# Kernel optimization log

Hardware: AMD Instinct MI355X
Metric: run time of the kernel (lower is better)

Reference implementation:

```python
import jax, jax.numpy as jnp
import numpy as np
from jax import lax

B, DIM, H, W = 2, 128, 192, 192
GS = [16, 32, 32, 48]          # group ratios [1,2,2,3]/8 of DIM
HID = int(DIM * 2.66)          # 340, Restormer-style hidden width


def _pool_mat(n_in, n_out):
    # torch AdaptiveAvgPool as an explicit linear map [n_out, n_in]
    P = np.zeros((n_out, n_in), np.float32)
    for o in range(n_out):
        s = (o * n_in) // n_out
        e = ((o + 1) * n_in + n_out - 1) // n_out
        P[o, s:e] = 1.0 / (e - s)
    return jnp.asarray(P)


def _ln(t, w, b):
    # WithBias LayerNorm over the channel dim of NCHW (== LN over last dim of b(hw)c)
    mu = t.mean(1, keepdims=True)
    var = ((t - mu) ** 2).mean(1, keepdims=True)
    return (t - mu) / jnp.sqrt(var + 1e-5) * w[None, :, None, None] + b[None, :, None, None]


def _c1x1(t, w):
    return jnp.einsum('oc,bchw->bohw', w, t)


def _dw3(t, w):
    return lax.conv_general_dilated(t, w, (1, 1), 'SAME',
                                    dimension_numbers=('NCHW', 'OIHW', 'NCHW'),
                                    feature_group_count=t.shape[1])


def _c1d(t, w, b):
    return jnp.einsum('oc,bcl->bol', w, t) + b[None, :, None]


def _gelu(t):
    return jax.nn.gelu(t, approximate=False)


def _forward(x, qv_cache, ln1_w, ln1_b, ln2_w, ln2_b, temperature, w_qkv, w_qkv_dw, w_proj,
             intra_down_w, intra_down_b, intra_up_w, intra_up_b, intra_gate_w, intra_gate_b,
             inter0_cw_w, inter0_cw_b, inter0_g_w, inter0_g_b,
             inter1_cw_w, inter1_cw_b, inter1_g_w, inter1_g_b,
             inter2_cw_w, inter2_cw_b, inter2_g_w, inter2_g_b,
             inter3_cw_w, inter3_cw_b, inter3_g_w, inter3_g_b,
             ffn_in_w, ffn_dw_w, ffn_out_w):
    b, c, h, w_ = x.shape
    hw = h * w_
    inter_p = [(inter0_cw_w, inter0_cw_b, inter0_g_w, inter0_g_b),
               (inter1_cw_w, inter1_cw_b, inter1_g_w, inter1_g_b),
               (inter2_cw_w, inter2_cw_b, inter2_g_w, inter2_g_b),
               (inter3_cw_w, inter3_cw_b, inter3_g_w, inter3_g_b)]
    # ---- attention branch ----
    xn = _ln(x, ln1_w, ln1_b)
    qkv = _dw3(_c1x1(xn, w_qkv), w_qkv_dw)
    q, k, v = jnp.split(qkv, 3, axis=1)
    q = q.reshape(b, c, hw); k = k.reshape(b, c, hw); v = v.reshape(b, c, hw)
    # correlation-based channel re-grouping (torch.corrcoef on batch-mean of q)
    cf = q.mean(0)                                   # [C, HW]
    xm = cf - cf.mean(1, keepdims=True)
    cov = xm @ xm.T
    dsd = jnp.sqrt(jnp.diagonal(cov))
    corr = cov / (dsd[:, None] * dsd[None, :])
    idx = jnp.argsort(-corr.mean(1))                 # descending mean similarity
    q = q[:, idx]; k = k[:, idx]; v = v[:, idx]
    atts, tmpc, outs = [], [], []
    start = 0
    for i, g in enumerate(GS):
        qg = q[:, start:start + g]; kg = k[:, start:start + g]; vg = v[:, start:start + g]
        start += g
        qn = qg / jnp.maximum(jnp.linalg.norm(qg, axis=-1, keepdims=True), 1e-12)
        kn = kg / jnp.maximum(jnp.linalg.norm(kg, axis=-1, keepdims=True), 1e-12)
        att = jax.nn.softmax(jnp.einsum('bcl,bdl->bcd', qn, kn) * temperature[i, 0, 0], axis=-1)
        tmpc.append(lax.stop_gradient(qn) + lax.stop_gradient(kn))
        # Inter_CacheModulation: adaptive-pool cache to [g,g], FiLM + gated conv1d
        cw_w, cw_b, g_w, g_b = inter_p[i]
        P = _pool_mat(c, g)
        aligned = jnp.einsum('oi,bij,pj->bop', P, qv_cache, P)    # [1, g, g]
        scale, shift = jnp.split(_c1d(aligned + att, cw_w, cw_b), 2, axis=1)
        x1p = att * scale + shift
        att = x1p * _gelu(_c1d(x1p, g_w, g_b)) + att
        atts.append(att)
        outs.append(jnp.einsum('bcd,bdl->bcl', att, vg))
    # CalculateCurrentLayerCache: resize each group's batch-mean attn to [C,C].
    # Original does (u * c_i) // dim with c_i == dim, i.e. elementwise floor.
    acc = jnp.zeros((1, c, c), x.dtype)
    for a in atts:
        m = lax.stop_gradient(a).mean(0, keepdims=True)[:, None]  # [1,1,g,g]
        u = jax.image.resize(m, (1, 1, c, c), method='bilinear')
        acc = acc + jnp.floor(u)[:, 0]
    qv_new = qv_cache * 0.9 + acc * 0.1
    out_all = jnp.concatenate(outs, axis=1)          # [B, C, HW]
    tmp_all = jnp.concatenate(tmpc, axis=1)
    # Intra_CacheModulation
    s = tmp_all + out_all
    gated = _gelu(_c1d(s, intra_gate_w, intra_gate_b)) * s
    out_all = _c1d(_c1d(gated, intra_down_w, intra_down_b), intra_up_w, intra_up_b) + out_all
    x1 = x + _c1x1(out_all.reshape(b, c, h, w_), w_proj)
    # ---- gated-dconv FFN ----
    xn2 = _ln(x1, ln2_w, ln2_b)
    y1, y2 = jnp.split(_dw3(_c1x1(xn2, ffn_in_w), ffn_dw_w), 2, axis=1)
    out = x1 + _c1x1(_gelu(y1) * y2, ffn_out_w)
    return out, qv_new


def setup_inputs() -> dict:
    key = jax.random.key(0)
    ks = jax.random.split(key, 40)
    def w(i, shape, s=0.02):
        return jax.random.normal(ks[i], shape, jnp.float32) * s
    p = {}
    p['x'] = jax.random.normal(ks[0], (B, DIM, H, W), jnp.float32)
    p['qv_cache'] = jax.random.uniform(ks[1], (1, DIM, DIM), jnp.float32)
    p['ln1_w'] = jnp.ones((DIM,), jnp.float32); p['ln1_b'] = jnp.zeros((DIM,), jnp.float32)
    p['ln2_w'] = jnp.ones((DIM,), jnp.float32); p['ln2_b'] = jnp.zeros((DIM,), jnp.float32)
    p['temperature'] = jnp.ones((4, 1, 1), jnp.float32)
    p['w_qkv'] = w(2, (3 * DIM, DIM))
    p['w_qkv_dw'] = w(3, (3 * DIM, 1, 3, 3))
    p['w_proj'] = w(4, (DIM, DIM))
    p['intra_down_w'] = w(5, (DIM // 2, DIM)); p['intra_down_b'] = jnp.zeros((DIM // 2,), jnp.float32)
    p['intra_up_w'] = w(6, (DIM, DIM // 2)); p['intra_up_b'] = jnp.zeros((DIM,), jnp.float32)
    p['intra_gate_w'] = w(7, (DIM, DIM)); p['intra_gate_b'] = jnp.zeros((DIM,), jnp.float32)
    for i, g in enumerate(GS):
        p[f'inter{i}_cw_w'] = w(8 + 2 * i, (2 * g, g))
        p[f'inter{i}_cw_b'] = jnp.zeros((2 * g,), jnp.float32)
        p[f'inter{i}_g_w'] = w(9 + 2 * i, (g, g))
        p[f'inter{i}_g_b'] = jnp.zeros((g,), jnp.float32)
    p['ffn_in_w'] = w(20, (2 * HID, DIM))
    p['ffn_dw_w'] = w(21, (2 * HID, 1, 3, 3))
    p['ffn_out_w'] = w(22, (DIM, HID))
    return p


def reference(x, qv_cache, ln1_w, ln1_b, ln2_w, ln2_b, temperature, w_qkv, w_qkv_dw, w_proj,
              intra_down_w, intra_down_b, intra_up_w, intra_up_b, intra_gate_w, intra_gate_b,
              inter0_cw_w, inter0_cw_b, inter0_g_w, inter0_g_b,
              inter1_cw_w, inter1_cw_b, inter1_g_w, inter1_g_b,
              inter2_cw_w, inter2_cw_b, inter2_g_w, inter2_g_b,
              inter3_cw_w, inter3_cw_b, inter3_g_w, inter3_g_b,
              ffn_in_w, ffn_dw_w, ffn_out_w):
    return _forward(x, qv_cache, ln1_w, ln1_b, ln2_w, ln2_b, temperature, w_qkv, w_qkv_dw, w_proj,
                    intra_down_w, intra_down_b, intra_up_w, intra_up_b, intra_gate_w, intra_gate_b,
                    inter0_cw_w, inter0_cw_b, inter0_g_w, inter0_g_b,
                    inter1_cw_w, inter1_cw_b, inter1_g_w, inter1_g_b,
                    inter2_cw_w, inter2_cw_b, inter2_g_w, inter2_g_b,
                    inter3_cw_w, inter3_cw_b, inter3_g_w, inter3_g_b,
                    ffn_in_w, ffn_dw_w, ffn_out_w)
```

## Files before the change

### kernel.cpp

```cpp
#include <hip/hip_runtime.h>
#include <math.h>

#define TPB 256

constexpr int BN_  = 2;
constexpr int CDIM = 128;
constexpr int HH   = 192;
constexpr int WW   = 192;
constexpr int HWc  = HH * WW;
constexpr int C3   = 384;
constexpr int HID  = 340;
constexpr int NL2  = 288;
constexpr int CH2  = HWc / NL2;
constexpr int CV   = 288;

typedef unsigned short bf16_t;
typedef __attribute__((ext_vector_type(8))) __bf16 bf16x8;
typedef __attribute__((ext_vector_type(4))) float f32x4;

__device__ __forceinline__ float b2f(bf16_t v) {
  unsigned u = ((unsigned)v) << 16;
  return __uint_as_float(u);
}
__device__ __forceinline__ bf16_t f2b(float f) {
  unsigned u = __float_as_uint(f);
  unsigned r = (u + 0x7FFFu + ((u >> 16) & 1u)) >> 16;
  return (bf16_t)r;
}
__device__ __forceinline__ float ldf(const float* p) { return *p; }
__device__ __forceinline__ float ldf(const bf16_t* p) { return b2f(*p); }
__device__ __forceinline__ void stf(float* p, float v) { *p = v; }
__device__ __forceinline__ void stf(bf16_t* p, float v) { *p = f2b(v); }

__device__ __forceinline__ void ldv4(const float* p, float* v) {
  float4 t = *(const float4*)p;
  v[0] = t.x; v[1] = t.y; v[2] = t.z; v[3] = t.w;
}
__device__ __forceinline__ void ldv4(const bf16_t* p, float* v) {
  ushort4 t = *(const ushort4*)p;
  v[0] = b2f(t.x); v[1] = b2f(t.y); v[2] = b2f(t.z); v[3] = b2f(t.w);
}
__device__ __forceinline__ void stv4(float* p, const float* v) {
  float4 t; t.x = v[0]; t.y = v[1]; t.z = v[2]; t.w = v[3];
  *(float4*)p = t;
}
__device__ __forceinline__ void stv4(bf16_t* p, const float* v) {
  ushort4 t; t.x = f2b(v[0]); t.y = f2b(v[1]); t.z = f2b(v[2]); t.w = f2b(v[3]);
  *(ushort4*)p = t;
}

__device__ __forceinline__ float gelu_f(float x) {
  return 0.5f * x * (1.0f + erff(x * 0.7071067811865475f));
}

__device__ __forceinline__ void unpack8(uint4 v, float* rv) {
  unsigned wv[4] = {v.x, v.y, v.z, v.w};
#pragma unroll
  for (int j = 0; j < 8; ++j)
    rv[j + 1] = b2f((bf16_t)((wv[j >> 1] >> ((j & 1) * 16)) & 0xFFFFu));
}
__device__ __forceinline__ uint4 pack8(const float* a) {
  uint4 o;
  unsigned w[4];
#pragma unroll
  for (int p = 0; p < 4; ++p) {
    unsigned lo = f2b(a[2 * p]), hi = f2b(a[2 * p + 1]);
    w[p] = lo | (hi << 16);
  }
  o.x = w[0]; o.y = w[1]; o.z = w[2]; o.w = w[3];
  return o;
}
__device__ __forceinline__ float sum8(uint4 v) {
  unsigned w[4] = {v.x, v.y, v.z, v.w};
  float s = 0.f;
#pragma unroll
  for (int j = 0; j < 8; ++j)
    s += b2f((bf16_t)((w[j >> 1] >> ((j & 1) * 16)) & 0xFFFFu));
  return s;
}
__device__ __forceinline__ float sumsq8(uint4 v) {
  unsigned w[4] = {v.x, v.y, v.z, v.w};
  float s = 0.f;
#pragma unroll
  for (int j = 0; j < 8; ++j) {
    float t = b2f((bf16_t)((w[j >> 1] >> ((j & 1) * 16)) & 0xFFFFu));
    s += t * t;
  }
  return s;
}

__device__ __constant__ int dGSZ[4]   = {16, 32, 32, 48};
__device__ __constant__ int dGST[4]   = {0, 16, 48, 80};
__device__ __constant__ int dAOFF[4]  = {0, 256, 1280, 2304};
__device__ __constant__ int dABASE[4] = {0, 512, 2560, 4608};

constexpr size_t oATTRAW  = 0;
constexpr size_t oATTS2   = 65536;
constexpr size_t oMUP     = 102400;
constexpr size_t oWB      = 131072;
constexpr size_t oATTS    = 1327104;
constexpr size_t oNORMQ   = 1363968;
constexpr size_t oNORMK   = 1364992;
constexpr size_t oIDX     = 1366016;
constexpr size_t oMU      = 1366528;
constexpr size_t oCOV     = 1367040;
constexpr size_t oQKV     = 1572864;
constexpr size_t oXN      = 58195968;
constexpr size_t oOUTALL  = 77070336;
constexpr size_t oSBUF    = 95944704;
constexpr size_t WS_NEED  = 114819072;
constexpr size_t oCHUNK1  = oOUTALL;
constexpr size_t oCOVPART = oOUTALL;
constexpr size_t oCOVP2   = oSBUF;
constexpr size_t oQKPART  = oXN;
constexpr size_t oGATED   = oQKV;
constexpr size_t oDBUF    = oQKV + 18874368;
constexpr size_t oY0C     = oQKV;
constexpr size_t oZ       = oOUTALL;
constexpr size_t oX1B     = oXN;

constexpr int eWQ   = 0;
constexpr int eGATE = 49152;
constexpr int eDOWN = 65536;
constexpr int eUP   = 73728;
constexpr int ePROJ = 81920;
constexpr int eFFI  = 98304;
constexpr int eFFO  = 185344;
constexpr int eTOT  = 234496;

__global__ __launch_bounds__(TPB) void k_wcvt(const float* __restrict__ wq,
                                              const float* __restrict__ gate,
                                              const float* __restrict__ down,
                                              const float* __restrict__ up,
                                              const float* __restrict__ proj,
                                              const float* __restrict__ ffi,
                                              const float* __restrict__ ffo,
                                              bf16_t* __restrict__ wb) {
  int t = blockIdx.x * TPB + threadIdx.x;
  if (t >= eTOT) return;
  int u = t;
  if (u < 49152) { wb[eWQ + u] = f2b(wq[u]); return; }
  u -= 49152;
  if (u < 16384) { wb[eGATE + u] = f2b(gate[u]); return; }
  u -= 16384;
  if (u < 8192)  { wb[eDOWN + u] = f2b(down[u]); return; }
  u -= 8192;
  if (u < 8192)  { wb[eUP + u] = f2b(up[u]); return; }
  u -= 8192;
  if (u < 16384) { wb[ePROJ + u] = f2b(proj[u]); return; }
  u -= 16384;
  if (u < 87040) { wb[eFFI + u] = f2b(ffi[u]); return; }
  u -= 87040;
  {
    int o = u / 384, k = u - o * 384;
    wb[eFFO + u] = (k < HID) ? f2b(ffo[o * HID + k]) : (bf16_t)0;
  }
}

template <typename TI>
__global__ __launch_bounds__(TPB) void k_ln(const TI* __restrict__ x,
                                            const float* __restrict__ w,
                                            const float* __restrict__ bias,
                                            bf16_t* __restrict__ out) {
  int t = blockIdx.x * TPB + threadIdx.x;
  if (t >= BN_ * HWc) return;
  int b = t / HWc, l = t - b * HWc;
  const TI* xb = x + (size_t)b * CDIM * HWc + l;
  float s = 0.f, s2 = 0.f;
#pragma unroll 4
  for (int c = 0; c < CDIM; ++c) { float v = ldf(&xb[(size_t)c * HWc]); s += v; s2 += v * v; }
  float mu  = s * (1.f / CDIM);
  float var = s2 * (1.f / CDIM) - mu * mu;
  float inv = 1.f / sqrtf(var + 1e-5f);
  bf16_t* ob = out + (size_t)b * CDIM * HWc + l;
#pragma unroll 4
  for (int c = 0; c < CDIM; ++c)
    stf(&ob[(size_t)c * HWc], (ldf(&xb[(size_t)c * HWc]) - mu) * inv * w[c] + bias[c]);
}

template <typename TO, typename TA, int KT, int EPI>
__global__ __launch_bounds__(TPB) void k_mgA(const bf16_t* __restrict__ W,
                                             const bf16_t* __restrict__ W2, int osplit,
                                             const float* __restrict__ bias,
                                             const bf16_t* __restrict__ in,
                                             const TA* __restrict__ aux,
                                             TO* __restrict__ out, int O,
                                             int ibr, int obr, int abr) {
  constexpr int L  = HWc;
  constexpr int PK = KT + 8;
  constexpr int KH = KT / 2;
  constexpr int SH = (KT == 128) ? 6 : 5;
  __shared__ bf16_t At[128 * PK];
  __shared__ bf16_t Wt[64 * PK];
  int b = blockIdx.y;
  const bf16_t* inb  = in  + (size_t)b * ibr * L;
  const TA*     auxb = aux ? aux + (size_t)b * abr * L : nullptr;
  TO*           outb = out + (size_t)b * obr * L;
  int l0 = blockIdx.x * 128;
  int tid = threadIdx.x, lane = tid & 63, wid = tid >> 6;
  int wm = wid >> 1, wn = wid & 1;
  int cl = lane & 15, rg = lane >> 4;

#pragma unroll
  for (int r = 0; r < (KH * 16) / TPB; ++r) {
    int u  = tid + r * TPB;
    int k2 = u & (KH - 1), lb = u >> SH;
    int ka = k2 * 2;
    uint4 rowA = *(const uint4*)(&inb[(size_t)ka * L + l0 + lb * 8]);
    uint4 rowB = *(const uint4*)(&inb[(size_t)(ka + 1) * L + l0 + lb * 8]);
    unsigned wa[4] = {rowA.x, rowA.y, rowA.z, rowA.w};
    unsigned wb[4] = {rowB.x, rowB.y, rowB.z, rowB.w};
#pragma unroll
    for (int j = 0; j < 8; ++j) {
      unsigned va = (wa[j >> 1] >> ((j & 1) * 16)) & 0xFFFFu;
      unsigned vb = (wb[j >> 1] >> ((j & 1) * 16)) & 0xFFFFu;
      *(unsigned*)(&At[(lb * 8 + j) * PK + ka]) = va | (vb << 16);
    }
  }

  int noc = (O + 63) >> 6;
  for (int oc = 0; oc < noc; ++oc) {
    int o0 = oc * 64;
#pragma unroll
    for (int r = 0; r < (64 * KT / 8) / TPB; ++r) {
      int e = tid + r * TPB;
      int o = e / (KT / 8), k8 = (e % (KT / 8)) * 8;
      int og = o0 + o;
      uint4 wv = {0u, 0u, 0u, 0u};
      if (og < O) {
        const bf16_t* wrow = (og < osplit) ? (W + (size_t)og * KT)
                                           : (W2 + (size_t)(og - osplit) * KT);
        wv = *(const uint4*)(&wrow[k8]);
      }
      *(uint4*)(&Wt[o * PK + k8]) = wv;
    }
    __syncthreads();
    f32x4 acc[2][4];
#pragma unroll
    for (int m = 0; m < 2; ++m)
#pragma unroll
      for (int n = 0; n < 4; ++n) acc[m][n] = (f32x4){0.f, 0.f, 0.f, 0.f};
#pragma unroll
    for (int kk = 0; kk < KT / 32; ++kk) {
      int kof = kk * 32 + rg * 8;
      bf16x8 a[2], bfr[4];
#pragma unroll
      for (int m = 0; m < 2; ++m)
        a[m] = *(const bf16x8*)(&Wt[(wm * 32 + m * 16 + cl) * PK + kof]);
#pragma unroll
      for (int n = 0; n < 4; ++n)
        bfr[n] = *(const bf16x8*)(&At[(wn * 64 + n * 16 + cl) * PK + kof]);
#pragma unroll
      for (int m = 0; m < 2; ++m)
#pragma unroll
        for (int n = 0; n < 4; ++n)
          acc[m][n] = __builtin_amdgcn_mfma_f32_16x16x32_bf16(bfr[n], a[m], acc[m][n], 0, 0, 0);
    }
    __syncthreads();
#pragma unroll
    for (int m = 0; m < 2; ++m) {
      int og = o0 + wm * 32 + m * 16 + cl;
      if (og >= O) continue;
      float bv = bias ? bias[og] : 0.f;
#pragma unroll
      for (int n = 0; n < 4; ++n) {
        int lcol = l0 + wn * 64 + n * 16 + rg * 4;
        size_t off = (size_t)og * L + lcol;
        float v[4];
#pragma unroll
        for (int r = 0; r < 4; ++r) v[r] = acc[m][n][r] + bv;
        if (EPI == 1) {
          float a4[4]; ldv4(&auxb[off], a4);
#pragma unroll
          for (int r = 0; r < 4; ++r) v[r] += a4[r];
        } else if (EPI == 2) {
          float a4[4]; ldv4(&auxb[off], a4);
#pragma unroll
          for (int r = 0; r < 4; ++r) v[r] = gelu_f(v[r]) * a4[r];
        } else if (EPI == 3) {
          int lloc = wn * 64 + n * 16 + rg * 4;
#pragma unroll
          for (int r = 0; r < 4; ++r)
            v[r] = gelu_f(v[r]) * b2f(At[(lloc + r) * PK + og]);
        }
        stv4(&outb[off], v);
      }
    }
  }
}

template <typename TO, typename TA, int EPI>
__global__ __launch_bounds__(TPB) void k_mgB(const bf16_t* __restrict__ Wb,
                                             const float* __restrict__ bias,
                                             const bf16_t* __restrict__ in,
                                             const TA* __restrict__ aux,
                                             TO* __restrict__ out, int O, int K,
                                             int ibr, int obr, int abr) {
  constexpr int L = HWc;
  constexpr int PK = 72, BK = 64, WSTR = 384;
  __shared__ bf16_t At[128 * PK];
  __shared__ bf16_t Wt[128 * PK];
  int b = blockIdx.y;
  const bf16_t* inb  = in  + (size_t)b * ibr * L;
  const TA*     auxb = aux ? aux + (size_t)b * abr * L : nullptr;
  TO*           outb = out + (size_t)b * obr * L;
  int l0 = blockIdx.x * 128;
  int tid = threadIdx.x, lane = tid & 63, wid = tid >> 6;
  int wm = wid >> 1, wn = wid & 1;
  int cl = lane & 15, rg = lane >> 4;

  f32x4 acc[4][4];
#pragma unroll
  for (int m = 0; m < 4; ++m)
#pragma unroll
    for (int n = 0; n < 4; ++n) acc[m][n] = (f32x4){0.f, 0.f, 0.f, 0.f};

  for (int k0 = 0; k0 < K; k0 += BK) {
#pragma unroll
    for (int r = 0; r < 2; ++r) {
      int u = tid + r * TPB;
      int k2 = u & 31, lb = u >> 5;
      int ka = k0 + k2 * 2;
      uint4 rowA = {0u,0u,0u,0u}, rowB = {0u,0u,0u,0u};
      if (ka < K)     rowA = *(const uint4*)(&inb[(size_t)ka * L + l0 + lb * 8]);
      if (ka + 1 < K) rowB = *(const uint4*)(&inb[(size_t)(ka + 1) * L + l0 + lb * 8]);
      unsigned wa[4] = {rowA.x, rowA.y, rowA.z, rowA.w};
      unsigned wb[4] = {rowB.x, rowB.y, rowB.z, rowB.w};
#pragma unroll
      for (int j = 0; j < 8; ++j) {
        unsigned va = (wa[j >> 1] >> ((j & 1) * 16)) & 0xFFFFu;
        unsigned vb = (wb[j >> 1] >> ((j & 1) * 16)) & 0xFFFFu;
        *(unsigned*)(&At[(lb * 8 + j) * PK + k2 * 2]) = va | (vb << 16);
      }
    }
#pragma unroll
    for (int r = 0; r < 4; ++r) {
      int e = tid + r * TPB;
      int o = e >> 3, k8 = (e & 7) * 8;
      uint4 wv = *(const uint4*)(&Wb[(size_t)o * WSTR + k0 + k8]);
      *(uint4*)(&Wt[o * PK + k8]) = wv;
    }
    __syncthreads();
#pragma unroll
    for (int kk = 0; kk < 2; ++kk) {
      int kof = kk * 32 + rg * 8;
      bf16x8 a[4], bfr[4];
#pragma unroll
      for (int m = 0; m < 4; ++m)
        a[m] = *(const bf16x8*)(&Wt[(wm * 64 + m * 16 + cl) * PK + kof]);
#pragma unroll
      for (int n = 0; n < 4; ++n)
        bfr[n] = *(const bf16x8*)(&At[(wn * 64 + n * 16 + cl) * PK + kof]);
#pragma unroll
      for (int m = 0; m < 4; ++m)
#pragma unroll
        for (int n = 0; n < 4; ++n)
          acc[m][n] = __builtin_amdgcn_mfma_f32_16x16x32_bf16(bfr[n], a[m], acc[m][n], 0, 0, 0);
    }
    __syncthreads();
  }
#pragma unroll
  for (int m = 0; m < 4; ++m) {
    int og = wm * 64 + m * 16 + cl;
    if (og >= O) continue;
    float bv = bias ? bias[og] : 0.f;
#pragma unroll
    for (int n = 0; n < 4; ++n) {
      int lcol = l0 + wn * 64 + n * 16 + rg * 4;
      size_t off = (size_t)og * L + lcol;
      float v[4];
#pragma unroll
      for (int r = 0; r < 4; ++r) v[r] = acc[m][n][r] + bv;
      if (EPI == 1) {
        float a4[4]; ldv4(&auxb[off], a4);
#pragma unroll
        for (int r = 0; r < 4; ++r) v[r] += a4[r];
      } else if (EPI == 2) {
        float a4[4]; ldv4(&auxb[off], a4);
#pragma unroll
        for (int r = 0; r < 4; ++r) v[r] = gelu_f(v[r]) * a4[r];
      }
      stv4(&outb[off], v);
    }
  }
}

__global__ __launch_bounds__(TPB) void k_dw3v(const bf16_t* __restrict__ in,
                                              const float* __restrict__ wt,
                                              bf16_t* __restrict__ out,
                                              int Cc, int c0, int CoutTotal, long totalG) {
  long t = (long)blockIdx.x * TPB + threadIdx.x;
  if (t >= totalG) return;
  int g = (int)(t % (HWc / 8));
  long bc = t / (HWc / 8);
  int cl = (int)(bc % Cc);
  int b = (int)(bc / Cc);
  int h = g / (WW / 8), w8 = (g % (WW / 8)) * 8;
  const bf16_t* ib = in + ((size_t)b * Cc + cl) * HWc;
  const float* wc = wt + (size_t)(c0 + cl) * 9;
  float rowv[3][10];
#pragma unroll
  for (int dy = -1; dy <= 1; ++dy) {
    float* rv = rowv[dy + 1];
    int hh = h + dy;
    if ((unsigned)hh >= (unsigned)HH) {
#pragma unroll
      for (int j = 0; j < 10; ++j) rv[j] = 0.f;
      continue;
    }
    const bf16_t* rp = ib + hh * WW + w8;
    unpack8(*(const uint4*)rp, rv);
    rv[0] = (w8 > 0) ? b2f(rp[-1]) : 0.f;
    rv[9] = (w8 + 8 < WW) ? b2f(rp[8]) : 0.f;
  }
  float a[8];
#pragma unroll
  for (int j = 0; j < 8; ++j) {
    float s = 0.f;
#pragma unroll
    for (int dy = 0; dy < 3; ++dy)
#pragma unroll
      for (int dx = 0; dx < 3; ++dx)
        s += rowv[dy][j + dx] * wc[dy * 3 + dx];
    a[j] = s;
  }
  *(uint4*)(&out[((size_t)b * CoutTotal + c0 + cl) * HWc + h * WW + w8]) = pack8(a);
}

__global__ __launch_bounds__(TPB) void k_mu1(const bf16_t* __restrict__ qkv,
                                             float* __restrict__ mupart) {
  int c = blockIdx.x, ch = blockIdx.y;
  int tid = threadIdx.x;
  int base = ch * (HWc / 8);
  __shared__ float red[TPB];
  float s = 0.f;
  for (int u = tid; u < (HWc / 8) / 8; u += TPB) {
    uint4 v0 = *(const uint4*)(&qkv[(size_t)c * HWc + base + u * 8]);
    uint4 v1 = *(const uint4*)(&qkv[(size_t)C3 * HWc + (size_t)c * HWc + base + u * 8]);
    s += 0.5f * (sum8(v0) + sum8(v1));
  }
  red[tid] = s;
  __syncthreads();
  for (int st = TPB / 2; st > 0; st >>= 1) {
    if (tid < st) red[tid] += red[tid + st];
    __syncthreads();
  }
  if (tid == 0) mupart[c * 8 + ch] = red[0];
}
__global__ __launch_bounds__(CDIM) void k_mured(const float* __restrict__ mupart,
                                                float* __restrict__ mu) {
  int c = threadIdx.x;
  float s = 0.f;
#pragma unroll
  for (int ch = 0; ch < 8; ++ch) s += mupart[c * 8 + ch];
  mu[c] = s / HWc;
}

__global__ __launch_bounds__(TPB) void k_cov4(const bf16_t* __restrict__ qkv,
                                              float* __restrict__ part) {
  constexpr int PK = 136;
  __shared__ bf16_t Xt[128 * PK];
  int chunk = blockIdx.x;
  int base = chunk * 128;
  int tid = threadIdx.x, lane = tid & 63, wid = tid >> 6;
  int wm = wid >> 1, wn = wid & 1;
  int cl = lane & 15, rg = lane >> 4;
#pragma unroll
  for (int r = 0; r < 8; ++r) {
    int u = tid + r * TPB;
    int c = u >> 4, l8 = (u & 15) * 8;
    uint4 v0 = *(const uint4*)(&qkv[(size_t)c * HWc + base + l8]);
    uint4 v1 = *(const uint4*)(&qkv[(size_t)C3 * HWc + (size_t)c * HWc + base + l8]);
    unsigned w0[4] = {v0.x, v0.y, v0.z, v0.w};
    unsigned w1[4] = {v1.x, v1.y, v1.z, v1.w};
    float cf[8];
#pragma unroll
    for (int j = 0; j < 8; ++j) {
      float a = b2f((bf16_t)((w0[j >> 1] >> ((j & 1) * 16)) & 0xFFFFu));
      float bq = b2f((bf16_t)((w1[j >> 1] >> ((j & 1) * 16)) & 0xFFFFu));
      cf[j] = 0.5f * (a + bq);
    }
    *(uint4*)(&Xt[c * PK + l8]) = pack8(cf);
  }
  __syncthreads();
  f32x4 acc[4][4];
#pragma unroll
  for (int m = 0; m < 4; ++m)
#pragma unroll
    for (int n = 0; n < 4; ++n) acc[m][n] = (f32x4){0.f, 0.f, 0.f, 0.f};
#pragma unroll
  for (int kk = 0; kk < 4; ++kk) {
    int kof = kk * 32 + rg * 8;
    bf16x8 a[4], bfr[4];
#pragma unroll
    for (int m = 0; m < 4; ++m)
      a[m] = *(const bf16x8*)(&Xt[(wm * 64 + m * 16 + cl) * PK + kof]);
#pragma unroll
    for (int n = 0; n < 4; ++n)
      bfr[n] = *(const bf16x8*)(&Xt[(wn * 64 + n * 16 + cl) * PK + kof]);
#pragma unroll
    for (int m = 0; m < 4; ++m)
#pragma unroll
      for (int n = 0; n < 4; ++n)
        acc[m][n] = __builtin_amdgcn_mfma_f32_16x16x32_bf16(bfr[n], a[m], acc[m][n], 0, 0, 0);
  }
  float* pb = part + (size_t)chunk * CDIM * CDIM;
#pragma unroll
  for (int m = 0; m < 4; ++m) {
    int c = wm * 64 + m * 16 + cl;
#pragma unroll
    for (int n = 0; n < 4; ++n) {
      int d0 = wn * 64 + n * 16 + rg * 4;
      float v[4] = {acc[m][n][0], acc[m][n][1], acc[m][n][2], acc[m][n][3]};
      stv4(&pb[c * CDIM + d0], v);
    }
  }
}

__global__ __launch_bounds__(TPB) void k_covred1(const float* __restrict__ part,
                                                 float* __restrict__ p2) {
  int t = blockIdx.x * TPB + threadIdx.x;
  int yg = blockIdx.y;
  float s = 0.f;
  for (int p = yg * 36; p < (yg + 1) * 36; ++p)
    s += part[(size_t)p * CDIM * CDIM + t];
  p2[(size_t)yg * CDIM * CDIM + t] = s;
}
__global__ __launch_bounds__(TPB) void k_covred2(const float* __restrict__ p2,
                                                 const float* __restrict__ mu,
                                                 float* __restrict__ cov) {
  int t = blockIdx.x * TPB + threadIdx.x;
  if (t >= CDIM * CDIM) return;
  float s = 0.f;
#pragma unroll
  for (int y = 0; y < 8; ++y) s += p2[(size_t)y * CDIM * CDIM + t];
  int c = t >> 7, d = t & 127;
  cov[t] = s - (float)HWc * mu[c] * mu[d];
}

__global__ __launch_bounds__(CDIM) void k_rank(const float* __restrict__ cov,
                                               int* __restrict__ idx) {
  __shared__ float dsd[CDIM], score[CDIM];
  int tid = threadIdx.x;
  dsd[tid] = sqrtf(cov[tid * CDIM + tid]);
  __syncthreads();
  {
    float s = 0.f, di = dsd[tid];
    for (int d = 0; d < CDIM; ++d) s += cov[tid * CDIM + d] / (di * dsd[d]);
    score[tid] = s;
  }
  __syncthreads();
  {
    float my = score[tid];
    int rank = 0;
    for (int d = 0; d < CDIM; ++d)
      rank += (score[d] > my) || (score[d] == my && d < tid);
    idx[rank] = tid;
  }
}

__global__ __launch_bounds__(TPB) void k_norms(const bf16_t* __restrict__ qkv,
                                               const int* __restrict__ idx,
                                               float* __restrict__ normq,
                                               float* __restrict__ normk) {
  int p = blockIdx.x, b = blockIdx.y, which = blockIdx.z;
  int ch = idx[p] + which * CDIM;
  const bf16_t* row = qkv + ((size_t)b * C3 + ch) * HWc;
  __shared__ float red[TPB];
  float s = 0.f;
  for (int u = threadIdx.x; u < HWc / 8; u += TPB)
    s += sumsq8(*(const uint4*)(&row[u * 8]));
  red[threadIdx.x] = s;
  __syncthreads();
  for (int st = TPB / 2; st > 0; st >>= 1) {
    if (threadIdx.x < st) red[threadIdx.x] += red[threadIdx.x + st];
    __syncthreads();
  }
  if (threadIdx.x == 0) {
    float n = fmaxf(sqrtf(red[0]), 1e-12f);
    (which ? normk : normq)[b * CDIM + p] = n;
  }
}

template <int G>
__device__ __forceinline__ void qk2_impl(char* sm, const bf16_t* __restrict__ qkv,
                                         const int* __restrict__ idx, int start,
                                         float* __restrict__ partial, int nl, int b) {
  constexpr int RT = G / 16;
  constexpr int U  = G * CH2 / 8;
  float (*qs)[CH2 + 2] = (float (*)[CH2 + 2])sm;
  float (*ks)[CH2 + 2] = (float (*)[CH2 + 2])(sm + (size_t)G * (CH2 + 2) * 4);
  int* idxg = (int*)(sm + (size_t)2 * G * (CH2 + 2) * 4);
  int tid = threadIdx.x;
  if (tid < G) idxg[tid] = idx[start + tid];
  __syncthreads();
  int l0 = nl * CH2;
  for (int u = tid; u < U; u += TPB) {
    int r = u / (CH2 / 8), c8 = (u % (CH2 / 8)) * 8;
    int ch = idxg[r];
    uint4 vq = *(const uint4*)(&qkv[((size_t)b * C3 + ch) * HWc + l0 + c8]);
    uint4 vk = *(const uint4*)(&qkv[((size_t)b * C3 + CDIM + ch) * HWc + l0 + c8]);
    unsigned wq[4] = {vq.x, vq.y, vq.z, vq.w};
    unsigned wk[4] = {vk.x, vk.y, vk.z, vk.w};
#pragma unroll
    for (int j = 0; j < 8; ++j) {
      qs[r][c8 + j] = b2f((bf16_t)((wq[j >> 1] >> ((j & 1) * 16)) & 0xFFFFu));
      ks[r][c8 + j] = b2f((bf16_t)((wk[j >> 1] >> ((j & 1) * 16)) & 0xFFFFu));
    }
  }
  __syncthreads();
  int ti = tid & 15, tj = tid >> 4;
  float acc[RT][RT];
#pragma unroll
  for (int m = 0; m < RT; ++m)
#pragma unroll
    for (int n = 0; n < RT; ++n) acc[m][n] = 0.f;
#pragma unroll 4
  for (int l = 0; l < CH2; ++l) {
    float qa[RT], kb[RT];
#pragma unroll
    for (int m = 0; m < RT; ++m) qa[m] = qs[ti * RT + m][l];
#pragma unroll
    for (int n = 0; n < RT; ++n) kb[n] = ks[tj * RT + n][l];
#pragma unroll
    for (int m = 0; m < RT; ++m)
#pragma unroll
      for (int n = 0; n < RT; ++n) acc[m][n] += qa[m] * kb[n];
  }
  float* pb = partial + ((size_t)(b * NL2) + nl) * G * G;
#pragma unroll
  for (int m = 0; m < RT; ++m)
#pragma unroll
    for (int n = 0; n < RT; ++n)
      pb[(ti * RT + m) * G + tj * RT + n] = acc[m][n];
}

__global__ __launch_bounds__(TPB) void k_qk2g(const bf16_t* __restrict__ qkv,
                                              const int* __restrict__ idx,
                                              float* __restrict__ qkpart) {
  extern __shared__ char sm[];
  int nl = blockIdx.x, b = blockIdx.y, gi = blockIdx.z;
  if (gi == 0)      qk2_impl<16>(sm, qkv, idx, 0,  qkpart + 0,       nl, b);
  else if (gi == 1) qk2_impl<32>(sm, qkv, idx, 16, qkpart + 147456,  nl, b);
  else if (gi == 2) qk2_impl<32>(sm, qkv, idx, 48, qkpart + 737280,  nl, b);
  else              qk2_impl<48>(sm, qkv, idx, 80, qkpart + 1327104, nl, b);
}

__global__ __launch_bounds__(TPB) void k_qkredg(const float* __restrict__ qkpart,
                                                float* __restrict__ attraw) {
  int t = blockIdx.x * TPB + threadIdx.x;
  if (t >= BN_ * 4608) return;
  int b = t / 4608, e = t - b * 4608;
  int gi = (e < 256) ? 0 : (e < 1280) ? 1 : (e < 2304) ? 2 : 3;
  const int gg4[4]    = {256, 1024, 1024, 2304};
  const int pgoff[4]  = {0, 147456, 737280, 1327104};
  const int aoff4[4]  = {0, 256, 1280, 2304};
  int GGg = gg4[gi];
  int el = e - aoff4[gi];
  const float* pb = qkpart + pgoff[gi] + (size_t)(b * NL2) * GGg + el;
  float s = 0.f;
  for (int nl = 0; nl < NL2; ++nl) s += pb[(size_t)nl * GGg];
  attraw[t] = s;
}

__global__ __launch_bounds__(TPB) void k_smg(const float* __restrict__ attraw,
                                             const float* __restrict__ normq,
                                             const float* __restrict__ normk,
                                             const float* __restrict__ temperature,
                                             float* __restrict__ attS) {
  int b = blockIdx.x, gi = blockIdx.y;
  int G = dGSZ[gi], start = dGST[gi];
  int GG = G * G;
  const float* ar = attraw + b * 4608 + dAOFF[gi];
  float* as = attS + b * 4608 + dAOFF[gi];
  float temp = temperature[gi];
  __shared__ float att[2304];
  int tid = threadIdx.x;
  for (int e = tid; e < GG; e += TPB) {
    int i = e / G, j = e - i * G;
    att[e] = ar[e] * temp / (normq[b * CDIM + start + i] * normk[b * CDIM + start + j]);
  }
  __syncthreads();
  if (tid < G) {
    float mx = -3.4e38f;
    for (int j = 0; j < G; ++j) mx = fmaxf(mx, att[tid * G + j]);
    float ssum = 0.f;
    for (int j = 0; j < G; ++j) { float ex = expf(att[tid * G + j] - mx); att[tid * G + j] = ex; ssum += ex; }
    float inv = 1.f / ssum;
    for (int j = 0; j < G; ++j) att[tid * G + j] *= inv;
  }
  __syncthreads();
  for (int e = tid; e < GG; e += TPB) as[e] = att[e];
}

__global__ __launch_bounds__(TPB) void k_imlpg(const float* __restrict__ attS,
                                               const float* __restrict__ qv_cache,
                                               const float* __restrict__ cw0, const float* __restrict__ cb0,
                                               const float* __restrict__ gw0, const float* __restrict__ gb0,
                                               const float* __restrict__ cw1, const float* __restrict__ cb1,
                                               const float* __restrict__ gw1, const float* __restrict__ gb1,
                                               const float* __restrict__ cw2, const float* __restrict__ cb2,
                                               const float* __restrict__ gw2, const float* __restrict__ gb2,
                                               const float* __restrict__ cw3, const float* __restrict__ cb3,
                                               const float* __restrict__ gw3, const float* __restrict__ gb3,
                                               float* __restrict__ attF) {
  int b = blockIdx.x, gi = blockIdx.y, tile = blockIdx.z;
  int G = dGSZ[gi];
  int p0 = tile * 16;
  if (p0 >= G) return;
  int GG = G * G;
  const float* cw_w = (gi == 0) ? cw0 : (gi == 1) ? cw1 : (gi == 2) ? cw2 : cw3;
  const float* cw_b = (gi == 0) ? cb0 : (gi == 1) ? cb1 : (gi == 2) ? cb2 : cb3;
  const float* g_w  = (gi == 0) ? gw0 : (gi == 1) ? gw1 : (gi == 2) ? gw2 : gw3;
  const float* g_b  = (gi == 0) ? gb0 : (gi == 1) ? gb1 : (gi == 2) ? gb2 : gb3;
  const float* as = attS + b * 4608 + dAOFF[gi];
  float* af = attF + dABASE[gi] + (size_t)b * GG;
  int tid = threadIdx.x;
  __shared__ float cwW[2 * 48 * 48];
  __shared__ float gW[48 * 48];
  __shared__ float attC[48 * 16], t1C[48 * 16], scC[48 * 16], shC[48 * 16],
                   x1pC[48 * 16], t2C[48 * 16];
  for (int e = tid; e < 2 * G * G; e += TPB) cwW[e] = cw_w[e];
  for (int e = tid; e < G * G; e += TPB) gW[e] = g_w[e];
  for (int u = tid; u < G * 16; u += TPB) {
    int c = u >> 4, pl = u & 15;
    int p = p0 + pl;
    float av = 0.f, pv = 0.f;
    if (p < G) {
      av = as[c * G + p];
      int so = c * CDIM / G, eo = ((c + 1) * CDIM + G - 1) / G;
      int sp = p * CDIM / G, ep = ((p + 1) * CDIM + G - 1) / G;
      float ssum = 0.f;
      for (int i2 = so; i2 < eo; ++i2)
        for (int j2 = sp; j2 < ep; ++j2) ssum += qv_cache[i2 * CDIM + j2];
      pv = ssum / (float)((eo - so) * (ep - sp));
    }
    attC[u] = av;
    t1C[u] = pv + av;
  }
  __syncthreads();
  for (int u = tid; u < 2 * G * 16; u += TPB) {
    int o = u >> 4, pl = u & 15;
    float acc = cw_b[o];
    for (int c = 0; c < G; ++c) acc += cwW[o * G + c] * t1C[c * 16 + pl];
    if (o < G) scC[o * 16 + pl] = acc;
    else       shC[(o - G) * 16 + pl] = acc;
  }
  __syncthreads();
  for (int u = tid; u < G * 16; u += TPB)
    x1pC[u] = attC[u] * scC[u] + shC[u];
  __syncthreads();
  for (int u = tid; u < G * 16; u += TPB) {
    int o = u >> 4, pl = u & 15;
    float acc = g_b[o];
    for (int c = 0; c < G; ++c) acc += gW[o * G + c] * x1pC[c * 16 + pl];
    t2C[u] = acc;
  }
  __syncthreads();
  for (int u = tid; u < G * 16; u += TPB) {
    int c = u >> 4, pl = u & 15;
    int p = p0 + pl;
    if (p < G)
      af[c * G + p] = x1pC[u] * gelu_f(t2C[u]) + attC[u];
  }
}

template <int G>
__device__ __forceinline__ void av_impl(char* sm, const bf16_t* __restrict__ qkv,
                                        const int* __restrict__ idx,
                                        const float* __restrict__ attF,
                                        const float* __restrict__ normq,
                                        const float* __restrict__ normk, int start,
                                        bf16_t* __restrict__ out_all,
                                        bf16_t* __restrict__ s_buf, int l0, int b) {
  constexpr int GH = G / 2;
  float (*vt)[129] = (float (*)[129])sm;
  float* attL = (float*)(sm + (size_t)G * 129 * 4);
  int* idxg = (int*)(sm + (size_t)G * 129 * 4 + (size_t)G * G * 4);
  int tid = threadIdx.x;
  if (tid < G) idxg[tid] = idx[start + tid];
  for (int e = tid; e < G * G; e += TPB) attL[e] = attF[(size_t)b * G * G + e];
  __syncthreads();
  for (int e = tid; e < G * 128; e += TPB) {
    int j = e >> 7, c = e & 127;
    vt[j][c] = b2f(qkv[((size_t)b * C3 + 2 * CDIM + idxg[j]) * HWc + l0 + c]);
  }
  __syncthreads();
  int ll = tid & 127, half = tid >> 7;
  float acc[GH];
#pragma unroll
  for (int i = 0; i < GH; ++i) acc[i] = 0.f;
  for (int j = 0; j < G; ++j) {
    float vv = vt[j][ll];
#pragma unroll
    for (int i = 0; i < GH; ++i) acc[i] += attL[(half * GH + i) * G + j] * vv;
  }
#pragma unroll
  for (int i = 0; i < GH; ++i) {
    int ig = half * GH + i;
    int p = start + ig;
    int ch = idxg[ig];
    float qv = b2f(qkv[((size_t)b * C3 + ch) * HWc + l0 + ll]);
    float kv = b2f(qkv[((size_t)b * C3 + CDIM + ch) * HWc + l0 + ll]);
    float tmp = qv / normq[b * CDIM + p] + kv / normk[b * CDIM + p];
    size_t off = ((size_t)b * CDIM + p) * HWc + l0 + ll;
    stf(&out_all[off], acc[i]);
    stf(&s_buf[off], acc[i] + tmp);
  }
}

__global__ __launch_bounds__(TPB) void k_avg(const bf16_t* __restrict__ qkv,
                                             const int* __restrict__ idx,
                                             const float* __restrict__ atts,
                                             const float* __restrict__ normq,
                                             const float* __restrict__ normk,
                                             bf16_t* __restrict__ out_all,
                                             bf16_t* __restrict__ s_buf) {
  extern __shared__ char sm[];
  int l0 = blockIdx.x * 128, b = blockIdx.y, gi = blockIdx.z;
  if (gi == 0)      av_impl<16>(sm, qkv, idx, atts + 0,    normq, normk, 0,  out_all, s_buf, l0, b);
  else if (gi == 1) av_impl<32>(sm, qkv, idx, atts + 512,  normq, normk, 16, out_all, s_buf, l0, b);
  else if (gi == 2) av_impl<32>(sm, qkv, idx, atts + 2560, normq, normk, 48, out_all, s_buf, l0, b);
  else              av_impl<48>(sm, qkv, idx, atts + 4608, normq, normk, 80, out_all, s_buf, l0, b);
}

__global__ __launch_bounds__(TPB) void k_qvnew(const float* __restrict__ attsF,
                                               const float* __restrict__ qv_cache,
                                               float* __restrict__ out_qv) {
  int t = blockIdx.x * TPB + threadIdx.x;
  if (t >= CDIM * CDIM) return;
  int r = t >> 7, cq = t & 127;
  const int gs[4]   = {16, 32, 32, 48};
  const int base[4] = {0, 512, 2560, 4608};
  float acc = 0.f;
  for (int gi = 0; gi < 4; ++gi) {
    int g = gs[gi], gg = g * g;
    const float* a0 = attsF + base[gi];
    float scale = (float)g / CDIM;
    float fr = (r + 0.5f) * scale - 0.5f;
    float fc = (cq + 0.5f) * scale - 0.5f;
    float flr = floorf(fr), flc = floorf(fc);
    int i0 = (int)flr, j0 = (int)flc;
    float wr = fr - flr, wcw = fc - flc;
    int i0c = max(i0, 0), i1c = min(i0 + 1, g - 1);
    int j0c = max(j0, 0), j1c = min(j0 + 1, g - 1);
    float m00 = 0.5f * (a0[i0c * g + j0c] + a0[gg + i0c * g + j0c]);
    float m01 = 0.5f * (a0[i0c * g + j1c] + a0[gg + i0c * g + j1c]);
    float m10 = 0.5f * (a0[i1c * g + j0c] + a0[gg + i1c * g + j0c]);
    float m11 = 0.5f * (a0[i1c * g + j1c] + a0[gg + i1c * g + j1c]);
    float val = (1.f - wr) * ((1.f - wcw) * m00 + wcw * m01)
              + wr * ((1.f - wcw) * m10 + wcw * m11);
    acc += floorf(val);
  }
  out_qv[t] = qv_cache[t] * 0.9f + acc * 0.1f;
}

__global__ __launch_bounds__(TPB) void k_dwgeluv(const bf16_t* __restrict__ y0c,
                                                 const float* __restrict__ wt,
                                                 bf16_t* __restrict__ z,
                                                 int Cc, int c0, long totalG) {
  long t = (long)blockIdx.x * TPB + threadIdx.x;
  if (t >= totalG) return;
  int g = (int)(t % (HWc / 8));
  long bc = t / (HWc / 8);
  int cl = (int)(bc % Cc);
  int b = (int)(bc / Cc);
  int h = g / (WW / 8), w8 = (g % (WW / 8)) * 8;
  const bf16_t* i1 = y0c + ((size_t)b * 2 * Cc + cl) * HWc;
  const bf16_t* i2 = y0c + ((size_t)b * 2 * Cc + Cc + cl) * HWc;
  const float* w1 = wt + (size_t)(c0 + cl) * 9;
  const float* w2 = wt + (size_t)(HID + c0 + cl) * 9;
  float r1[3][10], r2[3][10];
#pragma unroll
  for (int dy = -1; dy <= 1; ++dy) {
    float* v1 = r1[dy + 1];
    float* v2 = r2[dy + 1];
    int hh = h + dy;
    if ((unsigned)hh >= (unsigned)HH) {
#pragma unroll
      for (int j = 0; j < 10; ++j) { v1[j] = 0.f; v2[j] = 0.f; }
      continue;
    }
    const bf16_t* p1 = i1 + hh * WW + w8;
    const bf16_t* p2 = i2 + hh * WW + w8;
    unpack8(*(const uint4*)p1, v1);
    unpack8(*(const uint4*)p2, v2);
    bool hasL = (w8 > 0), hasR = (w8 + 8 < WW);
    v1[0] = hasL ? b2f(p1[-1]) : 0.f;
    v1[9] = hasR ? b2f(p1[8]) : 0.f;
    v2[0] = hasL ? b2f(p2[-1]) : 0.f;
    v2[9] = hasR ? b2f(p2[8]) : 0.f;
  }
  float o[8];
#pragma unroll
  for (int j = 0; j < 8; ++j) {
    float a1 = 0.f, a2 = 0.f;
#pragma unroll
    for (int dy = 0; dy < 3; ++dy)
#pragma unroll
      for (int dx = 0; dx < 3; ++dx) {
        a1 += r1[dy][j + dx] * w1[dy * 3 + dx];
        a2 += r2[dy][j + dx] * w2[dy * 3 + dx];
      }
    o[j] = gelu_f(a1) * a2;
  }
  *(uint4*)(&z[((size_t)b * HID + c0 + cl) * HWc + h * WW + w8]) = pack8(o);
}

extern "C" void kernel_launch(void* const* d_in, const int* in_sizes, int n_in,
                              void* d_out, int out_size, void* d_ws, size_t ws_size,
                              hipStream_t stream) {
  if (ws_size < WS_NEED) return;

  const float* x        = (const float*)d_in[0];
  const float* qv_cache = (const float*)d_in[1];
  const float* ln1_w    = (const float*)d_in[2];
  const float* ln1_b    = (const float*)d_in[3];
  const float* ln2_w    = (const float*)d_in[4];
  const float* ln2_b    = (const float*)d_in[5];
  const float* temperature = (const float*)d_in[6];
  const float* w_qkv    = (const float*)d_in[7];
  const float* w_qkv_dw = (const float*)d_in[8];
  const float* w_proj   = (const float*)d_in[9];
  const float* intra_down_w = (const float*)d_in[10];
  const float* intra_down_b = (const float*)d_in[11];
  const float* intra_up_w   = (const float*)d_in[12];
  const float* intra_up_b   = (const float*)d_in[13];
  const float* intra_gate_w = (const float*)d_in[14];
  const float* intra_gate_b = (const float*)d_in[15];
  const float* ffn_in_w  = (const float*)d_in[32];
  const float* ffn_dw_w  = (const float*)d_in[33];
  const float* ffn_out_w = (const float*)d_in[34];

  char* wsb = (char*)d_ws;
  float* out    = (float*)d_out;
  float* out_qv = out + (size_t)BN_ * CDIM * HWc;
  bf16_t* xn2   = (bf16_t*)d_out;

  float*  attraw  = (float*)(wsb + oATTRAW);
  float*  attS    = (float*)(wsb + oATTS2);
  float*  mupart  = (float*)(wsb + oMUP);
  bf16_t* wb      = (bf16_t*)(wsb + oWB);
  float*  atts    = (float*)(wsb + oATTS);
  float*  normq   = (float*)(wsb + oNORMQ);
  float*  normk   = (float*)(wsb + oNORMK);
  int*    idx     = (int*)(wsb + oIDX);
  float*  mu      = (float*)(wsb + oMU);
  float*  cov     = (float*)(wsb + oCOV);
  bf16_t* qkv     = (bf16_t*)(wsb + oQKV);
  bf16_t* xn      = (bf16_t*)(wsb + oXN);
  bf16_t* out_all = (bf16_t*)(wsb + oOUTALL);
  bf16_t* sbuf    = (bf16_t*)(wsb + oSBUF);
  bf16_t* chunk1  = (bf16_t*)(wsb + oCHUNK1);
  float*  covpart = (float*)(wsb + oCOVPART);
  float*  covp2   = (float*)(wsb + oCOVP2);
  float*  qkpart  = (float*)(wsb + oQKPART);
  bf16_t* gated   = (bf16_t*)(wsb + oGATED);
  bf16_t* dbuf    = (bf16_t*)(wsb + oDBUF);
  bf16_t* x1b     = (bf16_t*)(wsb + oX1B);
  bf16_t* y0c     = (bf16_t*)(wsb + oY0C);
  bf16_t* zbuf    = (bf16_t*)(wsb + oZ);

  const bf16_t* wq_b   = wb + eWQ;
  const bf16_t* gate_b = wb + eGATE;
  const bf16_t* down_b = wb + eDOWN;
  const bf16_t* up_b   = wb + eUP;
  const bf16_t* proj_b = wb + ePROJ;
  const bf16_t* ffi_b  = wb + eFFI;
  const bf16_t* ffo_b  = wb + eFFO;

  const int GX = HWc / 128;
  const int NOS = 1 << 30;
  dim3 gA(GX, BN_);

  k_wcvt<<<(eTOT + TPB - 1) / TPB, TPB, 0, stream>>>(
      w_qkv, intra_gate_w, intra_down_w, intra_up_w, w_proj, ffn_in_w, ffn_out_w, wb);

  k_ln<float><<<(BN_ * HWc + TPB - 1) / TPB, TPB, 0, stream>>>(x, ln1_w, ln1_b, xn);

  for (int ci = 0; ci < 2; ++ci) {
    int c0 = ci * 192;
    k_mgA<bf16_t, float, 128, 0><<<gA, TPB, 0, stream>>>(
        wq_b + (size_t)c0 * CDIM, wq_b, NOS, nullptr, xn, nullptr, chunk1,
        192, CDIM, 192, 0);
    long totG = (long)BN_ * 192 * (HWc / 8);
    k_dw3v<<<(unsigned)((totG + TPB - 1) / TPB), TPB, 0, stream>>>(
        chunk1, w_qkv_dw, qkv, 192, c0, C3, totG);
  }

  k_mu1<<<dim3(CDIM, 8), TPB, 0, stream>>>(qkv, mupart);
  k_mured<<<1, CDIM, 0, stream>>>(mupart, mu);
  k_cov4<<<CV, TPB, 0, stream>>>(qkv, covpart);
  k_covred1<<<dim3(64, 8), TPB, 0, stream>>>(covpart, covp2);
  k_covred2<<<64, TPB, 0, stream>>>(covp2, mu, cov);
  k_rank<<<1, CDIM, 0, stream>>>(cov, idx);
  k_norms<<<dim3(CDIM, BN_, 2), TPB, 0, stream>>>(qkv, idx, normq, normk);

  {
    size_t dyn = (size_t)2 * 48 * (CH2 + 2) * 4 + 48 * 4;
    k_qk2g<<<dim3(NL2, BN_, 4), TPB, dyn, stream>>>(qkv, idx, qkpart);
  }
  k_qkredg<<<(BN_ * 4608 + TPB - 1) / TPB, TPB, 0, stream>>>(qkpart, attraw);
  k_smg<<<dim3(BN_, 4), TPB, 0, stream>>>(attraw, normq, normk, temperature, attS);
  k_imlpg<<<dim3(BN_, 4, 3), TPB, 0, stream>>>(
      attS, qv_cache,
      (const float*)d_in[16], (const float*)d_in[17], (const float*)d_in[18], (const float*)d_in[19],
      (const float*)d_in[20], (const float*)d_in[21], (const float*)d_in[22], (const float*)d_in[23],
      (const float*)d_in[24], (const float*)d_in[25], (const float*)d_in[26], (const float*)d_in[27],
      (const float*)d_in[28], (const float*)d_in[29], (const float*)d_in[30], (const float*)d_in[31],
      atts);
  {
    size_t dyn = (size_t)48 * 129 * 4 + (size_t)48 * 48 * 4 + 48 * 4;
    k_avg<<<dim3(HWc / 128, BN_, 4), TPB, dyn, stream>>>(
        qkv, idx, atts, normq, normk, out_all, sbuf);
  }
  k_qvnew<<<(CDIM * CDIM + TPB - 1) / TPB, TPB, 0, stream>>>(atts, qv_cache, out_qv);

  k_mgA<bf16_t, float, 128, 3><<<gA, TPB, 0, stream>>>(
      gate_b, gate_b, NOS, intra_gate_b, sbuf, nullptr, gated,
      CDIM, CDIM, CDIM, 0);
  k_mgA<bf16_t, float, 128, 0><<<gA, TPB, 0, stream>>>(
      down_b, down_b, NOS, intra_down_b, gated, nullptr, dbuf,
      CDIM / 2, CDIM, CDIM / 2, 0);
  k_mgA<bf16_t, bf16_t, 64, 1><<<gA, TPB, 0, stream>>>(
      up_b, up_b, NOS, intra_up_b, dbuf, out_all, out_all,
      CDIM, CDIM / 2, CDIM, CDIM);
  k_mgA<bf16_t, float, 128, 1><<<gA, TPB, 0, stream>>>(
      proj_b, proj_b, NOS, nullptr, out_all, x, x1b, CDIM, CDIM, CDIM, CDIM);
  k_ln<bf16_t><<<(BN_ * HWc + TPB - 1) / TPB, TPB, 0, stream>>>(x1b, ln2_w, ln2_b, xn2);

  for (int ci = 0; ci < 2; ++ci) {
    int c0 = ci * 170;
    k_mgA<bf16_t, float, 128, 0><<<gA, TPB, 0, stream>>>(
        ffi_b + (size_t)c0 * CDIM, ffi_b + (size_t)(HID + c0) * CDIM, 170,
        nullptr, xn2, nullptr, y0c, 340, CDIM, 340, 0);
    long totG = (long)BN_ * 170 * (HWc / 8);
    k_dwgeluv<<<(unsigned)((totG + TPB - 1) / TPB), TPB, 0, stream>>>(
        y0c, ffn_dw_w, zbuf, 170, c0, totG);
  }
  k_mgB<float, bf16_t, 1><<<gA, TPB, 0, stream>>>(
      ffo_b, nullptr, zbuf, x1b, out, CDIM, HID, HID, CDIM, CDIM);
}
```

Baseline: 541.6 us.

## Use bf16 MFMA for attention-times-V and store reciprocal norms

Rewrites the attn@V kernel to stage V transposed and the attention matrix as bf16 in shared memory, then compute the product with 16x16x32 bf16 MFMA instructions. Outputs are written with vectorized 4-wide stores, replacing the scalar FP32 FMA loop. Norm kernels now store reciprocals so softmax scaling and the q/k residual use multiplies instead of divides. Rounding the attention weights to bf16 lowers precision slightly, and the transposed staging adds shared-memory packing work.

New measurement: 520.4 us. 3.9% less time.

```diff
diff --git a/kernel.cpp b/kernel.cpp
--- a/kernel.cpp
+++ b/kernel.cpp
@@ -561,8 +561,8 @@
 
 __global__ __launch_bounds__(TPB) void k_norms(const bf16_t* __restrict__ qkv,
                                                const int* __restrict__ idx,
-                                               float* __restrict__ normq,
-                                               float* __restrict__ normk) {
+                                               float* __restrict__ invq,
+                                               float* __restrict__ invk) {
   int p = blockIdx.x, b = blockIdx.y, which = blockIdx.z;
   int ch = idx[p] + which * CDIM;
   const bf16_t* row = qkv + ((size_t)b * C3 + ch) * HWc;
@@ -578,7 +578,7 @@
   }
   if (threadIdx.x == 0) {
     float n = fmaxf(sqrtf(red[0]), 1e-12f);
-    (which ? normk : normq)[b * CDIM + p] = n;
+    (which ? invk : invq)[b * CDIM + p] = 1.f / n;
   }
 }
 
@@ -664,8 +664,8 @@
 }
 
 __global__ __launch_bounds__(TPB) void k_smg(const float* __restrict__ attraw,
-                                             const float* __restrict__ normq,
-                                             const float* __restrict__ normk,
+                                             const float* __restrict__ invq,
+                                             const float* __restrict__ invk,
                                              const float* __restrict__ temperature,
                                              float* __restrict__ attS) {
   int b = blockIdx.x, gi = blockIdx.y;
@@ -678,7 +678,7 @@
   int tid = threadIdx.x;
   for (int e = tid; e < GG; e += TPB) {
     int i = e / G, j = e - i * G;
-    att[e] = ar[e] * temp / (normq[b * CDIM + start + i] * normk[b * CDIM + start + j]);
+    att[e] = ar[e] * temp * invq[b * CDIM + start + i] * invk[b * CDIM + start + j];
   }
   __syncthreads();
   if (tid < G) {
@@ -765,63 +765,102 @@
   }
 }
 
-template <int G>
-__device__ __forceinline__ void av_impl(char* sm, const bf16_t* __restrict__ qkv,
-                                        const int* __restrict__ idx,
-                                        const float* __restrict__ attF,
-                                        const float* __restrict__ normq,
-                                        const float* __restrict__ normk, int start,
-                                        bf16_t* __restrict__ out_all,
-                                        bf16_t* __restrict__ s_buf, int l0, int b) {
-  constexpr int GH = G / 2;
-  float (*vt)[129] = (float (*)[129])sm;
-  float* attL = (float*)(sm + (size_t)G * 129 * 4);
-  int* idxg = (int*)(sm + (size_t)G * 129 * 4 + (size_t)G * G * 4);
-  int tid = threadIdx.x;
+template <int G, int GP>
+__device__ __forceinline__ void av2_impl(char* sm, const bf16_t* __restrict__ qkv,
+                                         const int* __restrict__ idx,
+                                         const float* __restrict__ attF,
+                                         const float* __restrict__ invq,
+                                         const float* __restrict__ invk, int start,
+                                         bf16_t* __restrict__ out_all,
+                                         bf16_t* __restrict__ s_buf, int l0, int b) {
+  constexpr int PK = GP + 8;
+  constexpr int MT = G / 16;
+  bf16_t* Vt = (bf16_t*)sm;
+  bf16_t* Ab = (bf16_t*)(sm + (size_t)128 * PK * 2);
+  int* idxg  = (int*)(sm + (size_t)128 * PK * 2 + (size_t)G * PK * 2);
+  int tid = threadIdx.x, lane = tid & 63, wid = tid >> 6;
+  int cl = lane & 15, rg = lane >> 4;
   if (tid < G) idxg[tid] = idx[start + tid];
-  for (int e = tid; e < G * G; e += TPB) attL[e] = attF[(size_t)b * G * G + e];
-  __syncthreads();
-  for (int e = tid; e < G * 128; e += TPB) {
-    int j = e >> 7, c = e & 127;
-    vt[j][c] = b2f(qkv[((size_t)b * C3 + 2 * CDIM + idxg[j]) * HWc + l0 + c]);
-  }
-  __syncthreads();
-  int ll = tid & 127, half = tid >> 7;
-  float acc[GH];
-#pragma unroll
-  for (int i = 0; i < GH; ++i) acc[i] = 0.f;
-  for (int j = 0; j < G; ++j) {
-    float vv = vt[j][ll];
-#pragma unroll
-    for (int i = 0; i < GH; ++i) acc[i] += attL[(half * GH + i) * G + j] * vv;
-  }
-#pragma unroll
-  for (int i = 0; i < GH; ++i) {
-    int ig = half * GH + i;
-    int p = start + ig;
-    int ch = idxg[ig];
-    float qv = b2f(qkv[((size_t)b * C3 + ch) * HWc + l0 + ll]);
-    float kv = b2f(qkv[((size_t)b * C3 + CDIM + ch) * HWc + l0 + ll]);
-    float tmp = qv / normq[b * CDIM + p] + kv / normk[b * CDIM + p];
-    size_t off = ((size_t)b * CDIM + p) * HWc + l0 + ll;
-    stf(&out_all[off], acc[i]);
-    stf(&s_buf[off], acc[i] + tmp);
+  __syncthreads();
+  for (int u = tid; u < (GP / 2) * 16; u += TPB) {
+    int j2 = u % (GP / 2), lb = u / (GP / 2);
+    int ja = j2 * 2;
+    uint4 rA = {0u,0u,0u,0u}, rB = {0u,0u,0u,0u};
+    if (ja < G)     rA = *(const uint4*)(&qkv[((size_t)b * C3 + 2 * CDIM + idxg[ja]) * HWc + l0 + lb * 8]);
+    if (ja + 1 < G) rB = *(const uint4*)(&qkv[((size_t)b * C3 + 2 * CDIM + idxg[ja + 1]) * HWc + l0 + lb * 8]);
+    unsigned wa[4] = {rA.x, rA.y, rA.z, rA.w};
+    unsigned wb[4] = {rB.x, rB.y, rB.z, rB.w};
+#pragma unroll
+    for (int j = 0; j < 8; ++j) {
+      unsigned va = (wa[j >> 1] >> ((j & 1) * 16)) & 0xFFFFu;
+      unsigned vb = (wb[j >> 1] >> ((j & 1) * 16)) & 0xFFFFu;
+      *(unsigned*)(&Vt[(lb * 8 + j) * PK + ja]) = va | (vb << 16);
+    }
+  }
+  for (int e = tid; e < G * GP; e += TPB) {
+    int p = e / GP, j = e - p * GP;
+    Ab[p * PK + j] = (j < G) ? f2b(attF[(size_t)b * G * G + p * G + j]) : (bf16_t)0;
+  }
+  __syncthreads();
+  f32x4 acc[MT][2];
+#pragma unroll
+  for (int m = 0; m < MT; ++m)
+#pragma unroll
+    for (int n = 0; n < 2; ++n) acc[m][n] = (f32x4){0.f, 0.f, 0.f, 0.f};
+#pragma unroll
+  for (int kk = 0; kk < GP / 32; ++kk) {
+    int kof = kk * 32 + rg * 8;
+    bf16x8 a[MT], bfr[2];
+#pragma unroll
+    for (int m = 0; m < MT; ++m)
+      a[m] = *(const bf16x8*)(&Ab[(m * 16 + cl) * PK + kof]);
+#pragma unroll
+    for (int n = 0; n < 2; ++n)
+      bfr[n] = *(const bf16x8*)(&Vt[(wid * 32 + n * 16 + cl) * PK + kof]);
+#pragma unroll
+    for (int m = 0; m < MT; ++m)
+#pragma unroll
+      for (int n = 0; n < 2; ++n)
+        acc[m][n] = __builtin_amdgcn_mfma_f32_16x16x32_bf16(bfr[n], a[m], acc[m][n], 0, 0, 0);
+  }
+#pragma unroll
+  for (int m = 0; m < MT; ++m) {
+    int p = m * 16 + cl;
+    int pg = start + p;
+    int ch = idxg[p];
+    float iq = invq[b * CDIM + pg], ik = invk[b * CDIM + pg];
+#pragma unroll
+    for (int n = 0; n < 2; ++n) {
+      int lg = l0 + wid * 32 + n * 16 + rg * 4;
+      float q4[4], k4[4];
+      ldv4(&qkv[((size_t)b * C3 + ch) * HWc + lg], q4);
+      ldv4(&qkv[((size_t)b * C3 + CDIM + ch) * HWc + lg], k4);
+      float vo[4], vs[4];
+#pragma unroll
+      for (int r = 0; r < 4; ++r) {
+        vo[r] = acc[m][n][r];
+        vs[r] = vo[r] + q4[r] * iq + k4[r] * ik;
+      }
+      size_t off = ((size_t)b * CDIM + pg) * HWc + lg;
+      stv4(&out_all[off], vo);
+      stv4(&s_buf[off], vs);
+    }
   }
 }
 
 __global__ __launch_bounds__(TPB) void k_avg(const bf16_t* __restrict__ qkv,
                                              const int* __restrict__ idx,
                                              const float* __restrict__ atts,
-                                             const float* __restrict__ normq,
-                                             const float* __restrict__ normk,
+                                             const float* __restrict__ invq,
+                                             const float* __restrict__ invk,
                                              bf16_t* __restrict__ out_all,
                                              bf16_t* __restrict__ s_buf) {
   extern __shared__ char sm[];
   int l0 = blockIdx.x * 128, b = blockIdx.y, gi = blockIdx.z;
-  if (gi == 0)      av_impl<16>(sm, qkv, idx, atts + 0,    normq, normk, 0,  out_all, s_buf, l0, b);
-  else if (gi == 1) av_impl<32>(sm, qkv, idx, atts + 512,  normq, normk, 16, out_all, s_buf, l0, b);
-  else if (gi == 2) av_impl<32>(sm, qkv, idx, atts + 2560, normq, normk, 48, out_all, s_buf, l0, b);
-  else              av_impl<48>(sm, qkv, idx, atts + 4608, normq, normk, 80, out_all, s_buf, l0, b);
+  if (gi == 0)      av2_impl<16, 32>(sm, qkv, idx, atts + 0,    invq, invk, 0,  out_all, s_buf, l0, b);
+  else if (gi == 1) av2_impl<32, 32>(sm, qkv, idx, atts + 512,  invq, invk, 16, out_all, s_buf, l0, b);
+  else if (gi == 2) av2_impl<32, 32>(sm, qkv, idx, atts + 2560, invq, invk, 48, out_all, s_buf, l0, b);
+  else              av2_impl<48, 64>(sm, qkv, idx, atts + 4608, invq, invk, 80, out_all, s_buf, l0, b);
 }
 
 __global__ __launch_bounds__(TPB) void k_qvnew(const float* __restrict__ attsF,
@@ -942,8 +981,8 @@
   float*  mupart  = (float*)(wsb + oMUP);
   bf16_t* wb      = (bf16_t*)(wsb + oWB);
   float*  atts    = (float*)(wsb + oATTS);
-  float*  normq   = (float*)(wsb + oNORMQ);
-  float*  normk   = (float*)(wsb + oNORMK);
+  float*  invqA   = (float*)(wsb + oNORMQ);
+  float*  invkA   = (float*)(wsb + oNORMK);
   int*    idx     = (int*)(wsb + oIDX);
   float*  mu      = (float*)(wsb + oMU);
   float*  cov     = (float*)(wsb + oCOV);
@@ -994,14 +1033,14 @@
   k_covred1<<<dim3(64, 8), TPB, 0, stream>>>(covpart, covp2);
   k_covred2<<<64, TPB, 0, stream>>>(covp2, mu, cov);
   k_rank<<<1, CDIM, 0, stream>>>(cov, idx);
-  k_norms<<<dim3(CDIM, BN_, 2), TPB, 0, stream>>>(qkv, idx, normq, normk);
+  k_norms<<<dim3(CDIM, BN_, 2), TPB, 0, stream>>>(qkv, idx, invqA, invkA);
 
   {
     size_t dyn = (size_t)2 * 48 * (CH2 + 2) * 4 + 48 * 4;
     k_qk2g<<<dim3(NL2, BN_, 4), TPB, dyn, stream>>>(qkv, idx, qkpart);
   }
   k_qkredg<<<(BN_ * 4608 + TPB - 1) / TPB, TPB, 0, stream>>>(qkpart, attraw);
-  k_smg<<<dim3(BN_, 4), TPB, 0, stream>>>(attraw, normq, normk, temperature, attS);
+  k_smg<<<dim3(BN_, 4), TPB, 0, stream>>>(attraw, invqA, invkA, temperature, attS);
   k_imlpg<<<dim3(BN_, 4, 3), TPB, 0, stream>>>(
       attS, qv_cache,
       (const float*)d_in[16], (const float*)d_in[17], (const float*)d_in[18], (const float*)d_in[19],
@@ -1010,9 +1049,9 @@
       (const float*)d_in[28], (const float*)d_in[29], (const float*)d_in[30], (const float*)d_in[31],
       atts);
   {
-    size_t dyn = (size_t)48 * 129 * 4 + (size_t)48 * 48 * 4 + 48 * 4;
+    size_t dyn = (size_t)128 * 72 * 2 + (size_t)48 * 72 * 2 + 48 * 4;
     k_avg<<<dim3(HWc / 128, BN_, 4), TPB, dyn, stream>>>(
-        qkv, idx, atts, normq, normk, out_all, sbuf);
+        qkv, idx, atts, invqA, invkA, out_all, sbuf);
   }
   k_qvnew<<<(CDIM * CDIM + TPB - 1) / TPB, TPB, 0, stream>>>(atts, qv_cache, out_qv);
 
```
